# Kernel optimization log

Measured on AMD Instinct MI355X. Metric: run time of the kernel, lower is better.

Reference implementation:

```python
import jax, jax.numpy as jnp
import numpy as np

B, S, D, H = 4, 2048, 256, 8  # batch, seq (context=target), hidden_dim, n_heads


def setup_inputs() -> dict:
    key = jax.random.key(0)
    ks = jax.random.split(key, 12)
    sd = 1.0 / np.sqrt(D)          # torch Linear default init scale (uniform bound)
    sdo = 1.0 / np.sqrt(H * D)
    inp = {
        "k": jax.random.normal(ks[0], (B, S, D), jnp.float32),
        "v": jax.random.normal(ks[1], (B, S, D), jnp.float32),
        "q": jax.random.normal(ks[2], (B, S, D), jnp.float32),
        # Per-head projection weights, stacked over heads. Stored so y = x @ W + b.
        "Wk": jax.random.uniform(ks[3], (H, D, D), jnp.float32, -sd, sd),
        "bk": jax.random.uniform(ks[4], (H, D), jnp.float32, -sd, sd),
        "Wv": jax.random.uniform(ks[5], (H, D, D), jnp.float32, -sd, sd),
        "bv": jax.random.uniform(ks[6], (H, D), jnp.float32, -sd, sd),
        "Wq": jax.random.uniform(ks[7], (H, D, D), jnp.float32, -sd, sd),
        "bq": jax.random.uniform(ks[8], (H, D), jnp.float32, -sd, sd),
        # Final mixing Linear: input is heads interleaved as (hidden, head) flattened,
        # i.e. input index = hid * H + head (torch stack(dim=-1).view order).
        "Wo": jax.random.uniform(ks[9], (H * D, D), jnp.float32, -sdo, sdo),
        "bo": jax.random.uniform(ks[10], (D,), jnp.float32, -sdo, sdo),
    }
    return inp


def reference(k, v, q, Wk, bk, Wv, bv, Wq, bq, Wo, bo):
    # Per-head linear projections (batched over heads instead of a Python loop)
    k_ = jnp.einsum('bmd,hde->bhme', k, Wk) + bk[None, :, None, :]  # [B,H,S,D]
    v_ = jnp.einsum('bmd,hde->bhme', v, Wv) + bv[None, :, None, :]
    q_ = jnp.einsum('bnd,hde->bhne', q, Wq) + bq[None, :, None, :]
    scale = jnp.asarray(np.sqrt(D), k.dtype)
    # dot attention: scores[b,h,n,m] = <q_n, k_m> / sqrt(D); softmax over keys m
    scores = jnp.einsum('bhnd,bhmd->bhnm', q_, k_) / scale
    w = jax.nn.softmax(scores, axis=-1)
    rep = jnp.einsum('bhnm,bhmd->bhnd', w, v_)  # [B,H,S,D]
    # torch: stack(heads, dim=-1) -> [B,S,D,H], then view -> [B,S,D*H] (hid-major)
    outs = rep.transpose(0, 2, 3, 1).reshape(rep.shape[0], rep.shape[2], -1)
    return outs @ Wo + bo
```

## Files before the change

### kernel.cpp

```cpp
#include <hip/hip_runtime.h>

#define BB 4
#define SS 2048
#define DD 256
#define HH 8

typedef unsigned short u16;
typedef __attribute__((ext_vector_type(8))) short bf16x8;
typedef __attribute__((ext_vector_type(4))) float f32x4;
typedef __attribute__((ext_vector_type(16))) float f32x16;
typedef __attribute__((ext_vector_type(4))) short s16x4;

__device__ __forceinline__ f32x4 MFMA(bf16x8 a, bf16x8 b, f32x4 c) {
    return __builtin_amdgcn_mfma_f32_16x16x32_bf16(a, b, c, 0, 0, 0);
}
__device__ __forceinline__ f32x16 MFMA32(bf16x8 a, bf16x8 b, f32x16 c) {
    return __builtin_amdgcn_mfma_f32_32x32x16_bf16(a, b, c, 0, 0, 0);
}

__device__ __forceinline__ u16 f2bf_rtn(float x) {
    unsigned u = __float_as_uint(x);
    u += 0x7FFFu + ((u >> 16) & 1u);
    return (u16)(u >> 16);
}
__device__ __forceinline__ float bf2f(u16 h) {
    return __uint_as_float(((unsigned)h) << 16);
}
__device__ __forceinline__ void split2(float x, u16 &hi, u16 &lo) {
    hi = f2bf_rtn(x);
    lo = f2bf_rtn(x - bf2f(hi));
}

__device__ __forceinline__ void gl_lds16(const u16* g, u16* l) {
    __builtin_amdgcn_global_load_lds(
        (const __attribute__((address_space(1))) unsigned int*)(g),
        (__attribute__((address_space(3))) unsigned int*)(l), 16, 0, 0);
}

__global__ void prep_a(const float* __restrict__ x, u16* __restrict__ hi) {
    int r = blockIdx.x;
    int d = threadIdx.x;
    hi[(size_t)r * 256 + d] = f2bf_rtn(x[(size_t)r * 256 + d]);
}

__global__ void prep_w(const float* __restrict__ W, u16* __restrict__ Whi,
                       u16* __restrict__ Wlo) {
    int n = blockIdx.x;
    int h = n >> 8, e = n & 255;
    int d = threadIdx.x;
    float x = W[((size_t)h * 256 + d) * 256 + e];
    u16 hi, lo; split2(x, hi, lo);
    Whi[(size_t)n * 256 + d] = hi;
    Wlo[(size_t)n * 256 + d] = lo;
}

__global__ void prep_wo(const float* __restrict__ W, u16* __restrict__ Whi,
                        u16* __restrict__ Wlo) {
    int n = blockIdx.x;
    for (int k = threadIdx.x; k < 2048; k += 256) {
        int d = k & 255, h = k >> 8;
        float x = W[((size_t)(d * 8 + h)) * 256 + n];
        u16 hi, lo; split2(x, hi, lo);
        Whi[(size_t)n * 2048 + k] = hi;
        Wlo[(size_t)n * 2048 + k] = lo;
    }
}

template<int MODE, int AMODE, int TERMS, int BN, int LNXB>
__global__ __launch_bounds__(512, 2) void gemm_split(
    const u16* __restrict__ Ahi, const u16* __restrict__ Alo,
    const u16* __restrict__ Bhi, const u16* __restrict__ Blo,
    const float* __restrict__ bias,
    u16* __restrict__ Ohi,
    float* __restrict__ Of,
    int M, int N, int K, float scale)
{
    constexpr int WN = (BN == 128) ? 4 : 2;
    constexpr int WM = 8 / WN;
    constexpr int MSUB = (128 / WM) / 16;
    constexpr int NSUB = (BN / WN) / 16;
    constexpr int NPL = (TERMS == 3) ? 4 : (TERMS == 2) ? 3 : 2;

    __shared__ u16 lds[3 * NPL * 4096];

    const int tid = threadIdx.x;
    const int lane = tid & 63, wave = tid >> 6;
    const int wm = wave / WN, wn = wave % WN;
    const int cpx = (int)gridDim.x >> 3;
    const int wgs = (blockIdx.x & 7) * cpx + (blockIdx.x >> 3);
    const int m0 = (wgs >> LNXB) * 128;
    const int n0 = (wgs & ((1 << LNXB) - 1)) * BN;

    f32x4 acc[MSUB][NSUB];
#pragma unroll
    for (int i = 0; i < MSUB; ++i)
#pragma unroll
        for (int j = 0; j < NSUB; ++j) acc[i][j] = {0.f, 0.f, 0.f, 0.f};

    const int rho = tid >> 2;
    const int Xs = (tid & 3) << 3;
    const int ldsW = wave * 512;

#define G_ISSUE(k0v, p)                                                         \
    {   u16* Bse = lds + (p) * (NPL * 4096);                                    \
        size_t ga;                                                              \
        if (AMODE == 0)                                                         \
            ga = (size_t)(m0 + rho) * K + (k0v) + Xs;                           \
        else                                                                    \
            ga = ((size_t)((m0 >> 11) * 8 + ((k0v) >> 8)) * SS                  \
                  + (m0 & 2047) + rho) * DD + ((k0v) & 255) + Xs;               \
        gl_lds16(Ahi + ga, Bse + ldsW);                                         \
        if (TERMS == 3) gl_lds16(Alo + ga, Bse + 3 * 4096 + ldsW);              \
        if (BN == 128 || tid < 256) {                                           \
            size_t gb = (size_t)(n0 + rho) * K + (k0v) + Xs;                    \
            gl_lds16(Bhi + gb, Bse + 1 * 4096 + ldsW);                          \
            if (TERMS >= 2) gl_lds16(Blo + gb, Bse + 2 * 4096 + ldsW);          \
        }                                                                       \
    }

    const int NK = K >> 5;
    G_ISSUE(0, 0);
    G_ISSUE(32, 1);

    int buf = 0;
    for (int kt = 0; kt < NK; ++kt) {
        if (kt < NK - 1) {
            if (TERMS == 1)      { asm volatile("s_waitcnt vmcnt(2)" ::: "memory"); }
            else if (TERMS == 2) { asm volatile("s_waitcnt vmcnt(3)" ::: "memory"); }
            else {
                if (wave < 4) { asm volatile("s_waitcnt vmcnt(4)" ::: "memory"); }
                else          { asm volatile("s_waitcnt vmcnt(2)" ::: "memory"); }
            }
        } else {
            asm volatile("s_waitcnt vmcnt(0)" ::: "memory");
        }
        __builtin_amdgcn_sched_barrier(0);
        __builtin_amdgcn_s_barrier();
        __builtin_amdgcn_sched_barrier(0);

        if (kt + 2 < NK) {
            const int p2 = (buf + 2 >= 3) ? buf - 1 : buf + 2;
            G_ISSUE((kt + 2) << 5, p2);
        }

        const u16* Bse = lds + buf * (NPL * 4096);
        const int g8 = (lane >> 4) << 3;
        const int rA = wm * (128 / WM), rB = wn * (BN / WN);
        bf16x8 bh[NSUB], bl[NSUB];
#pragma unroll
        for (int ns = 0; ns < NSUB; ++ns) {
            const int rb = rB + ns * 16 + (lane & 15);
            bh[ns] = *(const bf16x8*)(Bse + 1 * 4096 + rb * 32 + g8);
            if (TERMS >= 2) bl[ns] = *(const bf16x8*)(Bse + 2 * 4096 + rb * 32 + g8);
        }
#pragma unroll
        for (int ms = 0; ms < MSUB; ++ms) {
            const int ra = rA + ms * 16 + (lane & 15);
            bf16x8 ah = *(const bf16x8*)(Bse + ra * 32 + g8);
            bf16x8 al;
            if (TERMS == 3) al = *(const bf16x8*)(Bse + 3 * 4096 + ra * 32 + g8);
#pragma unroll
            for (int ns = 0; ns < NSUB; ++ns) {
                acc[ms][ns] = MFMA(ah, bh[ns], acc[ms][ns]);
                if (TERMS == 3) acc[ms][ns] = MFMA(al, bh[ns], acc[ms][ns]);
                if (TERMS >= 2) acc[ms][ns] = MFMA(ah, bl[ns], acc[ms][ns]);
            }
        }
        buf = (buf + 1 == 3) ? 0 : buf + 1;
    }
#undef G_ISSUE

#pragma unroll
    for (int ms = 0; ms < MSUB; ++ms)
#pragma unroll
        for (int ns = 0; ns < NSUB; ++ns)
#pragma unroll
            for (int r = 0; r < 4; ++r) {
                int row = m0 + wm * (128 / WM) + ms * 16 + (lane >> 4) * 4 + r;
                int col = n0 + wn * (BN / WN) + ns * 16 + (lane & 15);
                float v = (acc[ms][ns][r] + bias[col]) * scale;
                if (MODE == 2) {
                    Of[(size_t)row * N + col] = v;
                } else {
                    int b = row >> 11, s = row & 2047, hh = col >> 8, e = col & 255;
                    size_t idx;
                    if (MODE == 0)
                        idx = ((size_t)(b * HH + hh) * SS + s) * DD + e;
                    else
                        idx = ((size_t)(b * HH + hh) * DD + e) * SS + s;
                    Ohi[idx] = f2bf_rtn(v);
                }
            }
}

__global__ __launch_bounds__(512, 2) void attn_kernel(
    const u16* __restrict__ Qhi,
    const u16* __restrict__ Khi,
    const u16* __restrict__ Vhi,
    u16* __restrict__ Rhi, u16* __restrict__ Rlo)
{
    __shared__ u16 lK[3][8192];
    __shared__ u16 lV[3][8192];

    const int tid = threadIdx.x, lane = tid & 63, wave = tid >> 6;
    const int qc = lane & 31, g2 = lane >> 5;
    const int wg = ((blockIdx.x & 7) << 5) + (blockIdx.x >> 3);
    const int bh = wg >> 3;
    const int qt = wg & 7;
    const size_t base = (size_t)bh * SS * DD;
    const int q0w = qt * 256 + wave * 32;

    bf16x8 qB[16];
#pragma unroll
    for (int ks = 0; ks < 16; ++ks)
        qB[ks] = *(const bf16x8*)(Qhi + base + (size_t)(q0w + qc) * DD + ks * 16 + g2 * 8);

    int koff[2], voff[2];
#pragma unroll
    for (int i = 0; i < 2; ++i) {
        const int s = tid + i * 512;
        const int kr = s >> 5, kX = s & 31;
        const int kap = (kr & 0x13) | ((kr & 4) << 1) | ((kr & 8) >> 1);
        koff[i] = kap * DD + ((kX ^ kr) << 3);
        const int ve = s >> 2, vXs = s & 3;
        voff[i] = ve * SS + (((vXs ^ ((ve >> 3) & 3))) << 3);
    }

    float l_part = 0.f;
    f32x16 acc[8];
#pragma unroll
    for (int ec = 0; ec < 8; ++ec) acc[ec] = {};

#define ISSUE(tt, p)                                                            \
    {   const u16* Kg = Khi + base + (size_t)(tt) * 32 * DD;                    \
        const u16* Vg = Vhi + base + (size_t)(tt) * 32;                         \
        u16* Kb = &lK[p][0]; u16* Vb = &lV[p][0];                               \
        gl_lds16(Kg + koff[0], Kb + wave * 512);                                \
        gl_lds16(Kg + koff[1], Kb + wave * 512 + 4096);                         \
        gl_lds16(Vg + voff[0], Vb + wave * 512);                                \
        gl_lds16(Vg + voff[1], Vb + wave * 512 + 4096);                         \
    }

    ISSUE(0, 0);
    ISSUE(1, 1);

    for (int t = 0; t < 64; ++t) {
        if (t < 63) { asm volatile("s_waitcnt vmcnt(4)" ::: "memory"); }
        else        { asm volatile("s_waitcnt vmcnt(0)" ::: "memory"); }
        __builtin_amdgcn_sched_barrier(0);
        __builtin_amdgcn_s_barrier();
        __builtin_amdgcn_sched_barrier(0);

        if (t + 2 < 64) ISSUE(t + 2, (t + 2) % 3);

        const u16* Kb = &lK[t % 3][0];
        const u16* Vb = &lV[t % 3][0];

        f32x16 sa = {}, sb = {};
        __builtin_amdgcn_s_setprio(1);
#pragma unroll
        for (int ks = 0; ks < 8; ++ks) {
            bf16x8 ka = *(const bf16x8*)(Kb + qc * DD + (((2 * ks + g2) ^ qc) << 3));
            bf16x8 kb2 = *(const bf16x8*)(Kb + qc * DD + (((2 * (ks + 8) + g2) ^ qc) << 3));
            sa = MFMA32(ka, qB[ks], sa);
            sb = MFMA32(kb2, qB[ks + 8], sb);
        }
        __builtin_amdgcn_s_setprio(0);

        f32x16 s = sa + sb;
#pragma unroll
        for (int n = 0; n < 16; ++n) s[n] = __builtin_amdgcn_exp2f(s[n] - 8.0f);
        float tl = 0.f;
#pragma unroll
        for (int n = 0; n < 16; ++n) tl += s[n];
        l_part += tl;

        bf16x8 p0, p1;
#pragma unroll
        for (int j = 0; j < 8; ++j) p0[j] = (short)f2bf_rtn(s[j]);
#pragma unroll
        for (int j = 0; j < 8; ++j) p1[j] = (short)f2bf_rtn(s[8 + j]);

        __builtin_amdgcn_s_setprio(1);
#pragma unroll
        for (int ec = 0; ec < 8; ++ec) {
            const int e = ec * 32 + qc;
            bf16x8 v0 = *(const bf16x8*)(Vb + e * 32 + (((g2 ^ ((e >> 3) & 3))) << 3));
            bf16x8 v1 = *(const bf16x8*)(Vb + e * 32 + ((((2 + g2) ^ ((e >> 3) & 3))) << 3));
            acc[ec] = MFMA32(v0, p0, acc[ec]);
            acc[ec] = MFMA32(v1, p1, acc[ec]);
        }
        __builtin_amdgcn_s_setprio(0);
    }
#undef ISSUE

    float l = l_part + __shfl_xor(l_part, 32);
    float inv = 1.0f / l;
    const size_t rowbase = ((size_t)bh * SS + q0w + qc) * DD;
#pragma unroll
    for (int ec = 0; ec < 8; ++ec)
#pragma unroll
        for (int rr = 0; rr < 4; ++rr) {
            const int e0 = ec * 32 + 8 * rr + 4 * g2;
            s16x4 hv, lv;
#pragma unroll
            for (int j = 0; j < 4; ++j) {
                u16 h2, l2; split2(acc[ec][4 * rr + j] * inv, h2, l2);
                hv[j] = (short)h2; lv[j] = (short)l2;
            }
            *(s16x4*)(Rhi + rowbase + e0) = hv;
            *(s16x4*)(Rlo + rowbase + e0) = lv;
        }
}

extern "C" void kernel_launch(void* const* d_in, const int* in_sizes, int n_in,
                              void* d_out, int out_size, void* d_ws, size_t ws_size,
                              hipStream_t stream)
{
    (void)in_sizes; (void)n_in; (void)out_size; (void)ws_size;
    const float* k_in = (const float*)d_in[0];
    const float* v_in = (const float*)d_in[1];
    const float* q_in = (const float*)d_in[2];
    const float* Wk   = (const float*)d_in[3];
    const float* bk   = (const float*)d_in[4];
    const float* Wv   = (const float*)d_in[5];
    const float* bv   = (const float*)d_in[6];
    const float* Wq   = (const float*)d_in[7];
    const float* bq   = (const float*)d_in[8];
    const float* Wo   = (const float*)d_in[9];
    const float* bo   = (const float*)d_in[10];
    float* out = (float*)d_out;

    char* p = (char*)d_ws;
    const size_t MB = 1024 * 1024;
    u16* WqH = (u16*)(p + 0 * MB);
    u16* WqL = (u16*)(p + 1 * MB);
    u16* WkH = (u16*)(p + 2 * MB);
    u16* WkL = (u16*)(p + 3 * MB);
    u16* WvH = (u16*)(p + 4 * MB);
    u16* WvL = (u16*)(p + 5 * MB);
    u16* WoH = (u16*)(p + 6 * MB);
    u16* WoL = (u16*)(p + 7 * MB);
    const size_t PB = 32 * MB;
    u16* QH  = (u16*)(p + 8 * MB);
    u16* KH  = (u16*)(p + 8 * MB + 1 * PB);
    u16* VTH = (u16*)(p + 8 * MB + 2 * PB);
    u16* RH  = (u16*)(p + 8 * MB + 3 * PB);
    u16* RL  = (u16*)(p + 8 * MB + 4 * PB);
    u16* AqH = (u16*)(p + 168 * MB);
    u16* AkH = (u16*)(p + 172 * MB);
    u16* AvH = (u16*)(p + 176 * MB);

    prep_a<<<dim3(8192), dim3(256), 0, stream>>>(q_in, AqH);
    prep_a<<<dim3(8192), dim3(256), 0, stream>>>(k_in, AkH);
    prep_a<<<dim3(8192), dim3(256), 0, stream>>>(v_in, AvH);
    prep_w<<<dim3(2048), dim3(256), 0, stream>>>(Wq, WqH, WqL);
    prep_w<<<dim3(2048), dim3(256), 0, stream>>>(Wk, WkH, WkL);
    prep_w<<<dim3(2048), dim3(256), 0, stream>>>(Wv, WvH, WvL);
    prep_wo<<<dim3(256), dim3(256), 0, stream>>>(Wo, WoH, WoL);

    const float qscale = 1.4426950408889634f / 16.0f;
    gemm_split<0, 0, 1, 128, 4><<<dim3(1024), dim3(512), 0, stream>>>(
        AqH, nullptr, WqH, WqL, bq, QH, nullptr, 8192, 2048, 256, qscale);
    gemm_split<0, 0, 1, 128, 4><<<dim3(1024), dim3(512), 0, stream>>>(
        AkH, nullptr, WkH, WkL, bk, KH, nullptr, 8192, 2048, 256, 1.0f);
    gemm_split<1, 0, 2, 128, 4><<<dim3(1024), dim3(512), 0, stream>>>(
        AvH, nullptr, WvH, WvL, bv, VTH, nullptr, 8192, 2048, 256, 1.0f);

    attn_kernel<<<dim3(256), dim3(512), 0, stream>>>(
        QH, KH, VTH, RH, RL);

    gemm_split<2, 2, 3, 64, 2><<<dim3(256), dim3(512), 0, stream>>>(
        RH, RL, WoH, WoL, bo, nullptr, out, 8192, 256, 2048, 1.0f);
}
```

Before: 297.6 us.

## Split-K the output projection GEMM and truncate attention probabilities to bf16

The final output-projection GEMM (K=2048) now runs as a two-way split-K over 512 workgroups instead of 256, with double buffering for the split case. Each half writes fp32 partials into scratch, and a new reduce kernel sums them and adds the bias. This fills more CUs in the last stage at the cost of an extra kernel launch and a round trip of partials through global memory. Separately, the softmax probabilities are converted to bf16 by truncation with packed bit ops instead of round-to-nearest, which cuts ALU work but adds a small rounding bias.

```diff
diff --git a/kernel.cpp b/kernel.cpp
--- a/kernel.cpp
+++ b/kernel.cpp
@@ -66,7 +66,16 @@
     }
 }
 
-template<int MODE, int AMODE, int TERMS, int BN, int LNXB>
+__global__ void reduce_out(const float* __restrict__ P, const float* __restrict__ bias,
+                           float* __restrict__ out) {
+    const int i = blockIdx.x * 1024 + threadIdx.x * 4;
+    f32x4 a = *(const f32x4*)(P + i);
+    f32x4 b = *(const f32x4*)(P + 2097152 + i);
+    f32x4 bv = *(const f32x4*)(bias + ((threadIdx.x * 4) & 255));
+    *(f32x4*)(out + i) = (a + b) + bv;
+}
+
+template<int MODE, int AMODE, int TERMS, int BN, int LNXB, int SPLK>
 __global__ __launch_bounds__(512, 2) void gemm_split(
     const u16* __restrict__ Ahi, const u16* __restrict__ Alo,
     const u16* __restrict__ Bhi, const u16* __restrict__ Blo,
@@ -80,16 +89,21 @@
     constexpr int MSUB = (128 / WM) / 16;
     constexpr int NSUB = (BN / WN) / 16;
     constexpr int NPL = (TERMS == 3) ? 4 : (TERMS == 2) ? 3 : 2;
-
-    __shared__ u16 lds[3 * NPL * 4096];
+    constexpr int NBUF = SPLK ? 2 : 3;
+
+    __shared__ u16 lds[NBUF * NPL * 4096];
 
     const int tid = threadIdx.x;
     const int lane = tid & 63, wave = tid >> 6;
     const int wm = wave / WN, wn = wave % WN;
-    const int cpx = (int)gridDim.x >> 3;
-    const int wgs = (blockIdx.x & 7) * cpx + (blockIdx.x >> 3);
+    const int nwg = (int)gridDim.x >> SPLK;
+    const int kc = SPLK ? (blockIdx.x >= (unsigned)nwg ? 1 : 0) : 0;
+    const int b2 = SPLK ? ((int)blockIdx.x - kc * nwg) : (int)blockIdx.x;
+    const int cpx = nwg >> 3;
+    const int wgs = (b2 & 7) * cpx + (b2 >> 3);
     const int m0 = (wgs >> LNXB) * 128;
     const int n0 = (wgs & ((1 << LNXB) - 1)) * BN;
+    const int kb = kc * (K >> SPLK);
 
     f32x4 acc[MSUB][NSUB];
 #pragma unroll
@@ -118,18 +132,22 @@
         }                                                                       \
     }
 
-    const int NK = K >> 5;
-    G_ISSUE(0, 0);
-    G_ISSUE(32, 1);
+    const int NK = (K >> 5) >> SPLK;
+    G_ISSUE(kb, 0);
+    if (NBUF == 3) G_ISSUE(kb + 32, 1);
 
     int buf = 0;
     for (int kt = 0; kt < NK; ++kt) {
-        if (kt < NK - 1) {
-            if (TERMS == 1)      { asm volatile("s_waitcnt vmcnt(2)" ::: "memory"); }
-            else if (TERMS == 2) { asm volatile("s_waitcnt vmcnt(3)" ::: "memory"); }
-            else {
-                if (wave < 4) { asm volatile("s_waitcnt vmcnt(4)" ::: "memory"); }
-                else          { asm volatile("s_waitcnt vmcnt(2)" ::: "memory"); }
+        if (NBUF == 3) {
+            if (kt < NK - 1) {
+                if (TERMS == 1)      { asm volatile("s_waitcnt vmcnt(2)" ::: "memory"); }
+                else if (TERMS == 2) { asm volatile("s_waitcnt vmcnt(3)" ::: "memory"); }
+                else {
+                    if (wave < 4) { asm volatile("s_waitcnt vmcnt(4)" ::: "memory"); }
+                    else          { asm volatile("s_waitcnt vmcnt(2)" ::: "memory"); }
+                }
+            } else {
+                asm volatile("s_waitcnt vmcnt(0)" ::: "memory");
             }
         } else {
             asm volatile("s_waitcnt vmcnt(0)" ::: "memory");
@@ -138,9 +156,13 @@
         __builtin_amdgcn_s_barrier();
         __builtin_amdgcn_sched_barrier(0);
 
-        if (kt + 2 < NK) {
-            const int p2 = (buf + 2 >= 3) ? buf - 1 : buf + 2;
-            G_ISSUE((kt + 2) << 5, p2);
+        if (NBUF == 3) {
+            if (kt + 2 < NK) {
+                const int p2 = (buf + 2 >= 3) ? buf - 1 : buf + 2;
+                G_ISSUE(kb + ((kt + 2) << 5), p2);
+            }
+        } else {
+            if (kt + 1 < NK) G_ISSUE(kb + ((kt + 1) << 5), (kt + 1) & 1);
         }
 
         const u16* Bse = lds + buf * (NPL * 4096);
@@ -166,7 +188,7 @@
                 if (TERMS >= 2) acc[ms][ns] = MFMA(ah, bl[ns], acc[ms][ns]);
             }
         }
-        buf = (buf + 1 == 3) ? 0 : buf + 1;
+        buf = (buf + 1 == NBUF) ? 0 : buf + 1;
     }
 #undef G_ISSUE
 
@@ -178,17 +200,22 @@
             for (int r = 0; r < 4; ++r) {
                 int row = m0 + wm * (128 / WM) + ms * 16 + (lane >> 4) * 4 + r;
                 int col = n0 + wn * (BN / WN) + ns * 16 + (lane & 15);
-                float v = (acc[ms][ns][r] + bias[col]) * scale;
-                if (MODE == 2) {
-                    Of[(size_t)row * N + col] = v;
+                if (MODE == 3) {
+                    Of[(size_t)kc * ((size_t)M * N) + (size_t)row * N + col] =
+                        acc[ms][ns][r];
                 } else {
-                    int b = row >> 11, s = row & 2047, hh = col >> 8, e = col & 255;
-                    size_t idx;
-                    if (MODE == 0)
-                        idx = ((size_t)(b * HH + hh) * SS + s) * DD + e;
-                    else
-                        idx = ((size_t)(b * HH + hh) * DD + e) * SS + s;
-                    Ohi[idx] = f2bf_rtn(v);
+                    float v = (acc[ms][ns][r] + bias[col]) * scale;
+                    if (MODE == 2) {
+                        Of[(size_t)row * N + col] = v;
+                    } else {
+                        int b = row >> 11, s = row & 2047, hh = col >> 8, e = col & 255;
+                        size_t idx;
+                        if (MODE == 0)
+                            idx = ((size_t)(b * HH + hh) * SS + s) * DD + e;
+                        else
+                            idx = ((size_t)(b * HH + hh) * DD + e) * SS + s;
+                        Ohi[idx] = f2bf_rtn(v);
+                    }
                 }
             }
 }
@@ -277,9 +304,14 @@
 
         bf16x8 p0, p1;
 #pragma unroll
-        for (int j = 0; j < 8; ++j) p0[j] = (short)f2bf_rtn(s[j]);
-#pragma unroll
-        for (int j = 0; j < 8; ++j) p1[j] = (short)f2bf_rtn(s[8 + j]);
+        for (int j = 0; j < 4; ++j) {
+            unsigned a = __float_as_uint(s[2 * j]);
+            unsigned b = __float_as_uint(s[2 * j + 1]);
+            ((unsigned*)&p0)[j] = (a >> 16) | (b & 0xffff0000u);
+            unsigned c = __float_as_uint(s[8 + 2 * j]);
+            unsigned d = __float_as_uint(s[8 + 2 * j + 1]);
+            ((unsigned*)&p1)[j] = (c >> 16) | (d & 0xffff0000u);
+        }
 
         __builtin_amdgcn_s_setprio(1);
 #pragma unroll
@@ -350,6 +382,7 @@
     u16* AqH = (u16*)(p + 168 * MB);
     u16* AkH = (u16*)(p + 172 * MB);
     u16* AvH = (u16*)(p + 176 * MB);
+    float* Pf = (float*)(p + 8 * MB);
 
     prep_a<<<dim3(8192), dim3(256), 0, stream>>>(q_in, AqH);
     prep_a<<<dim3(8192), dim3(256), 0, stream>>>(k_in, AkH);
@@ -360,16 +393,17 @@
     prep_wo<<<dim3(256), dim3(256), 0, stream>>>(Wo, WoH, WoL);
 
     const float qscale = 1.4426950408889634f / 16.0f;
-    gemm_split<0, 0, 1, 128, 4><<<dim3(1024), dim3(512), 0, stream>>>(
+    gemm_split<0, 0, 1, 128, 4, 0><<<dim3(1024), dim3(512), 0, stream>>>(
         AqH, nullptr, WqH, WqL, bq, QH, nullptr, 8192, 2048, 256, qscale);
-    gemm_split<0, 0, 1, 128, 4><<<dim3(1024), dim3(512), 0, stream>>>(
+    gemm_split<0, 0, 1, 128, 4, 0><<<dim3(1024), dim3(512), 0, stream>>>(
         AkH, nullptr, WkH, WkL, bk, KH, nullptr, 8192, 2048, 256, 1.0f);
-    gemm_split<1, 0, 2, 128, 4><<<dim3(1024), dim3(512), 0, stream>>>(
+    gemm_split<1, 0, 2, 128, 4, 0><<<dim3(1024), dim3(512), 0, stream>>>(
         AvH, nullptr, WvH, WvL, bv, VTH, nullptr, 8192, 2048, 256, 1.0f);
 
     attn_kernel<<<dim3(256), dim3(512), 0, stream>>>(
         QH, KH, VTH, RH, RL);
 
-    gemm_split<2, 2, 3, 64, 2><<<dim3(256), dim3(512), 0, stream>>>(
-        RH, RL, WoH, WoL, bo, nullptr, out, 8192, 256, 2048, 1.0f);
-}
+    gemm_split<3, 2, 3, 64, 2, 1><<<dim3(512), dim3(512), 0, stream>>>(
+        RH, RL, WoH, WoL, bo, nullptr, Pf, 8192, 256, 2048, 1.0f);
+    reduce_out<<<dim3(2048), dim3(256), 0, stream>>>(Pf, bo, out);
+}
```

Result: faster. 291.0 us (-2.2%).
